# Optimization experiments

Measured on AMD Instinct MI355X. Metric: run time of the kernel, lower is better.

Reference implementation:

```python
import jax, jax.numpy as jnp
import numpy as np

D_IN = 1024
D_OUT = 1024


def setup_inputs() -> dict:
    key = jax.random.key(0)
    kx, kq, kk, kv = jax.random.split(key, 4)
    x = jax.random.normal(kx, (4, 2048, D_IN), dtype=jnp.float32)
    s = 1.0 / np.sqrt(D_IN)
    Wq = jax.random.normal(kq, (D_IN, D_OUT), dtype=jnp.float32) * s
    Wk = jax.random.normal(kk, (D_IN, D_OUT), dtype=jnp.float32) * s
    Wv = jax.random.normal(kv, (D_IN, D_OUT), dtype=jnp.float32) * s
    return {"x": x, "Wq": Wq, "Wk": Wk, "Wv": Wv}


def reference(x, Wq, Wk, Wv):
    # x: [B, S, d_in]; W*: [d_in, d_out]
    B, S, _ = x.shape
    q = x @ Wq  # [B, S, d_out]
    k = x @ Wk
    v = x @ Wv
    scale = 1.0 / jnp.sqrt(jnp.asarray(k.shape[-1], x.dtype))
    scores = jnp.einsum("bqd,bkd->bqk", q, k) * scale  # [B, S, S]
    # causal mask: positions j > i masked to -inf (triu, diagonal=1)
    causal = jnp.tril(jnp.ones((S, S), dtype=bool))
    scores = jnp.where(causal[None, :, :], scores, -jnp.inf)
    attn = jax.nn.softmax(scores, axis=-1)  # dropout p=0.0 -> identity
    return jnp.einsum("bqk,bkd->bqd", attn, v)
```

## Files before the change

kernel.cpp:

```cpp
#include <hip/hip_runtime.h>
#include <hip/hip_bf16.h>

#define NB 4
#define SB 2048
#define DD 1024
#define BM 128
#define BN 128
#define BK 32

typedef __attribute__((ext_vector_type(8))) short bf16x8;
typedef __attribute__((ext_vector_type(4))) short bf16x4;
typedef __attribute__((ext_vector_type(4))) float f32x4;
typedef unsigned int u32;

__device__ __forceinline__ float bf2f(unsigned short u) {
    return __uint_as_float(((u32)u) << 16);
}
__device__ __forceinline__ short f2bf(float f) {
    u32 u = __float_as_uint(f);
    u32 r = (u + 0x7fffu + ((u >> 16) & 1u)) >> 16;
    return (short)r;
}

__global__ __launch_bounds__(256) void prep(
    const float* __restrict__ x, const float* __restrict__ Wq,
    const float* __restrict__ Wk, const float* __restrict__ Wv,
    short* __restrict__ xb, short* __restrict__ Wqb,
    short* __restrict__ Wkb, short* __restrict__ Wvt)
{
    __shared__ short t[64][65];
    const int bx = blockIdx.x;
    const int tid = threadIdx.x;
    if (bx < 5120) {
        const float* src;
        short* dst;
        size_t i;
        if (bx < 4096) {
            src = x; dst = xb;
            i = ((size_t)bx * 256 + tid) * 8;
        } else {
            const int w = bx - 4096;
            src = (w < 512) ? Wq : Wk;
            dst = (w < 512) ? Wqb : Wkb;
            i = ((size_t)(w & 511) * 256 + tid) * 8;
        }
        float4 a = *(const float4*)&src[i];
        float4 b = *(const float4*)&src[i + 4];
        bf16x8 o;
        o[0] = f2bf(a.x); o[1] = f2bf(a.y); o[2] = f2bf(a.z); o[3] = f2bf(a.w);
        o[4] = f2bf(b.x); o[5] = f2bf(b.y); o[6] = f2bf(b.z); o[7] = f2bf(b.w);
        *(bf16x8*)&dst[i] = o;
        return;
    }
    const int rr = bx - 5120;
    const int k0 = (rr & 15) * 64;
    const int n0 = (rr >> 4) * 64;
    {
        const int r = tid >> 4;
        const int c = (tid & 15) * 4;
#pragma unroll
        for (int i = 0; i < 4; i++) {
            float4 v = *(const float4*)&Wv[(size_t)(k0 + i * 16 + r) * DD + n0 + c];
            t[i * 16 + r][c + 0] = f2bf(v.x);
            t[i * 16 + r][c + 1] = f2bf(v.y);
            t[i * 16 + r][c + 2] = f2bf(v.z);
            t[i * 16 + r][c + 3] = f2bf(v.w);
        }
    }
    __syncthreads();
    {
        const int r = tid >> 3;
        const int c = (tid & 7) * 8;
#pragma unroll
        for (int i = 0; i < 2; i++) {
            bf16x8 o;
#pragma unroll
            for (int j = 0; j < 8; j++) o[j] = t[c + j][i * 32 + r];
            *(bf16x8*)&Wvt[(size_t)(n0 + i * 32 + r) * DD + k0 + c] = o;
        }
    }
}

__device__ __forceinline__ void stage128x32(const short* __restrict__ g, int ld,
                                            short* lds, int tid) {
    const int wave = tid >> 6, lane = tid & 63;
    const int r = lane >> 2;
    const int c = (lane & 3) * 8;
#pragma unroll
    for (int i = 0; i < 2; i++) {
        const int chunk = wave * 2 + i;
        const short* gp = g + (size_t)(chunk * 16 + r) * ld + c;
        __builtin_amdgcn_global_load_lds(
            (const __attribute__((address_space(1))) u32*)gp,
            (__attribute__((address_space(3))) u32*)(lds + chunk * 512 + lane * 8),
            16, 0, 0);
    }
}

__device__ __forceinline__ void gemm_bt_body(
    const short* __restrict__ A, int lda, const short* __restrict__ Bt, int ldb,
    int m0, int n0, int kend, short* As, short* Bs, f32x4 (&acc)[4][4], int tid)
{
    const int lane = tid & 63;
    const int wave = tid >> 6;
    const int wm = (wave >> 1) * 64, wn = (wave & 1) * 64;
    const int fr = lane & 15;
    const int quad = lane >> 4;
    for (int k0 = 0; k0 < kend; k0 += BK) {
        stage128x32(A + (size_t)m0 * lda + k0, lda, As, tid);
        stage128x32(Bt + (size_t)n0 * ldb + k0, ldb, Bs, tid);
        __syncthreads();
        bf16x8 af[4], bf[4];
#pragma unroll
        for (int t = 0; t < 4; t++) {
            af[t] = *(const bf16x8*)&As[(wm + t * 16 + fr) * BK + quad * 8];
            bf[t] = *(const bf16x8*)&Bs[(wn + t * 16 + fr) * BK + quad * 8];
        }
#pragma unroll
        for (int mt = 0; mt < 4; mt++)
#pragma unroll
            for (int nt = 0; nt < 4; nt++)
                acc[mt][nt] = __builtin_amdgcn_mfma_f32_16x16x32_bf16(
                    af[mt], bf[nt], acc[mt][nt], 0, 0, 0);
        __syncthreads();
    }
}

__global__ __launch_bounds__(256) void mm_kernel(
    const short* __restrict__ Wkb, const short* __restrict__ Wqb,
    short* __restrict__ Mp)
{
    __shared__ short As[BM * BK], Bs[BN * BK];
    const int n0 = blockIdx.x * BN;
    const int m0 = blockIdx.y * BM;
    f32x4 acc[4][4];
#pragma unroll
    for (int a = 0; a < 4; a++)
#pragma unroll
        for (int b = 0; b < 4; b++) acc[a][b] = (f32x4){0.f, 0.f, 0.f, 0.f};
    gemm_bt_body(Wkb, DD, Wqb, DD, m0, n0, DD, As, Bs, acc, threadIdx.x);
    const int lane = threadIdx.x & 63, wave = threadIdx.x >> 6;
    const int wm = (wave >> 1) * 64, wn = (wave & 1) * 64;
    const int fr = lane & 15, quad = lane >> 4;
#pragma unroll
    for (int mt = 0; mt < 4; mt++)
#pragma unroll
        for (int nt = 0; nt < 4; nt++)
#pragma unroll
            for (int r = 0; r < 4; r++) {
                const size_t m = m0 + wm + mt * 16 + quad * 4 + r;
                const size_t n = n0 + wn + nt * 16 + fr;
                Mp[m * DD + n] = f2bf(acc[mt][nt][r]);
            }
}

__global__ __launch_bounds__(256) void tv_gemm(
    const short* __restrict__ xb, const short* __restrict__ Mp,
    const short* __restrict__ Wvt, short* __restrict__ T,
    short* __restrict__ Vt)
{
    __shared__ short As[BM * BK], Bs[BN * BK];
    const int n0 = blockIdx.x * BN;
    const int m0 = blockIdx.y * BM;
    const int z = blockIdx.z;
    const short* B = (z == 0) ? Mp : Wvt;
    f32x4 acc[4][4];
#pragma unroll
    for (int a = 0; a < 4; a++)
#pragma unroll
        for (int b = 0; b < 4; b++) acc[a][b] = (f32x4){0.f, 0.f, 0.f, 0.f};
    gemm_bt_body(xb, DD, B, DD, m0, n0, DD, As, Bs, acc, threadIdx.x);
    const int lane = threadIdx.x & 63, wave = threadIdx.x >> 6;
    const int wm = (wave >> 1) * 64, wn = (wave & 1) * 64;
    const int fr = lane & 15, quad = lane >> 4;
    if (z == 0) {
#pragma unroll
        for (int mt = 0; mt < 4; mt++)
#pragma unroll
            for (int nt = 0; nt < 4; nt++)
#pragma unroll
                for (int r = 0; r < 4; r++) {
                    const size_t m = m0 + wm + mt * 16 + quad * 4 + r;
                    const size_t n = n0 + wn + nt * 16 + fr;
                    T[m * DD + n] = f2bf(acc[mt][nt][r]);
                }
    } else {
        const int bb = m0 >> 11;
        const int s0 = (m0 & (SB - 1)) + wm + quad * 4;
        short* Vb = Vt + (size_t)bb * DD * SB;
#pragma unroll
        for (int mt = 0; mt < 4; mt++)
#pragma unroll
            for (int nt = 0; nt < 4; nt++) {
                const size_t n = n0 + wn + nt * 16 + fr;
                const size_t s = s0 + mt * 16;
                bf16x4 o;
#pragma unroll
                for (int r = 0; r < 4; r++) o[r] = f2bf(acc[mt][nt][r]);
                *(bf16x4*)&Vb[n * SB + s] = o;
            }
    }
}

__global__ __launch_bounds__(256) void scores_mfma(
    const short* __restrict__ T, const short* __restrict__ xb,
    short* __restrict__ Sc)
{
    const int idx = blockIdx.x;
    int qt = (int)((__fsqrt_rn(8.f * idx + 1.f) - 1.f) * 0.5f);
    while ((qt + 1) * (qt + 2) / 2 <= idx) qt++;
    while (qt * (qt + 1) / 2 > idx) qt--;
    const int kt = idx - qt * (qt + 1) / 2;
    const int qm0 = qt * BM;
    const int kn0 = kt * BN;
    const int b = blockIdx.y;
    __shared__ short As[BM * BK], Bs[BN * BK];
    const short* Tb = T + (size_t)b * SB * DD;
    const short* Xb = xb + (size_t)b * SB * DD;
    short* Sb = Sc + (size_t)b * SB * SB;
    f32x4 acc[4][4];
#pragma unroll
    for (int a = 0; a < 4; a++)
#pragma unroll
        for (int c = 0; c < 4; c++) acc[a][c] = (f32x4){0.f, 0.f, 0.f, 0.f};
    gemm_bt_body(Tb, DD, Xb, DD, qm0, kn0, DD, As, Bs, acc, threadIdx.x);
    const int lane = threadIdx.x & 63, wave = threadIdx.x >> 6;
    const int wm = (wave >> 1) * 64, wn = (wave & 1) * 64;
    const int fr = lane & 15, quad = lane >> 4;
    const float scale = 0.03125f;
#pragma unroll
    for (int mt = 0; mt < 4; mt++)
#pragma unroll
        for (int nt = 0; nt < 4; nt++)
#pragma unroll
            for (int r = 0; r < 4; r++) {
                const size_t q = qm0 + wm + mt * 16 + quad * 4 + r;
                const size_t k = kn0 + wn + nt * 16 + fr;
                Sb[q * SB + k] = f2bf(acc[mt][nt][r] * scale);
            }
}

__global__ __launch_bounds__(256) void softmax_kernel(short* __restrict__ Sc)
{
    const int row = blockIdx.x;
    const int i = row & (SB - 1);
    const int jlim = ((i >> 7) + 1) << 7;
    short* r = Sc + (size_t)row * SB;
    const int t = threadIdx.x;
    const int lane = t & 63, wave = t >> 6;
    __shared__ float red[8];

    float v[8];
    float mx = -1e30f;
#pragma unroll
    for (int c = 0; c < 8; c++) {
        const int j = c * 256 + t;
        const float s = (j <= i) ? bf2f((unsigned short)r[j]) : -1e30f;
        v[c] = s;
        mx = fmaxf(mx, s);
    }
#pragma unroll
    for (int o = 32; o > 0; o >>= 1) mx = fmaxf(mx, __shfl_down(mx, o));
    if (lane == 0) red[wave] = mx;
    __syncthreads();
    mx = fmaxf(fmaxf(red[0], red[1]), fmaxf(red[2], red[3]));

    float sum = 0.f;
#pragma unroll
    for (int c = 0; c < 8; c++) {
        const int j = c * 256 + t;
        const float e = (j <= i) ? __expf(v[c] - mx) : 0.f;
        v[c] = e;
        sum += e;
    }
#pragma unroll
    for (int o = 32; o > 0; o >>= 1) sum += __shfl_down(sum, o);
    if (lane == 0) red[4 + wave] = sum;
    __syncthreads();
    const float inv = 1.0f / (red[4] + red[5] + red[6] + red[7]);
#pragma unroll
    for (int c = 0; c < 8; c++) {
        const int j = c * 256 + t;
        if (j < jlim) r[j] = f2bf(v[c] * inv);
    }
}

__global__ __launch_bounds__(256) void pv_mfma(
    const short* __restrict__ P, const short* __restrict__ Vt,
    float* __restrict__ O, float* __restrict__ Pp)
{
    __shared__ short As[BM * BK], Bs[BN * BK];
    const int n0 = blockIdx.x * BN;
    const int y = blockIdx.y;
    const int chunk1 = (y >= 16);
    const int qt = chunk1 ? (y - 8) : y;
    const int qm0 = qt * BM;
    const int kstart = chunk1 ? 1024 : 0;
    const int kstop = chunk1 ? (qt + 1) * BM : min(1024, (qt + 1) * BM);
    const int b = blockIdx.z;
    const short* Pb = P + (size_t)b * SB * SB + kstart;
    const short* Vb = Vt + (size_t)b * DD * SB + kstart;
    f32x4 acc[4][4];
#pragma unroll
    for (int a = 0; a < 4; a++)
#pragma unroll
        for (int c = 0; c < 4; c++) acc[a][c] = (f32x4){0.f, 0.f, 0.f, 0.f};
    gemm_bt_body(Pb, SB, Vb, SB, qm0, n0, kstop - kstart, As, Bs, acc,
                 threadIdx.x);
    const int lane = threadIdx.x & 63, wave = threadIdx.x >> 6;
    const int wm = (wave >> 1) * 64, wn = (wave & 1) * 64;
    const int fr = lane & 15, quad = lane >> 4;
    float* dst = chunk1 ? (Pp + (size_t)b * 1024 * DD)
                        : (O + (size_t)b * SB * DD);
    const int qoff = chunk1 ? 1024 : 0;
#pragma unroll
    for (int mt = 0; mt < 4; mt++)
#pragma unroll
        for (int nt = 0; nt < 4; nt++)
#pragma unroll
            for (int r = 0; r < 4; r++) {
                const size_t q = qm0 + wm + mt * 16 + quad * 4 + r - qoff;
                const size_t n = n0 + wn + nt * 16 + fr;
                dst[q * DD + n] = acc[mt][nt][r];
            }
}

__global__ __launch_bounds__(256) void reduce_pv(const float* __restrict__ Pp,
                                                 float* __restrict__ O)
{
    const size_t e = ((size_t)blockIdx.x * 256 + threadIdx.x) * 4;
    const size_t b = e / ((size_t)1024 * DD);
    const size_t rem = e - b * (size_t)1024 * DD;
    float4 p = *(const float4*)&Pp[e];
    float* o = &O[b * (size_t)SB * DD + (size_t)1024 * DD + rem];
    float4 v = *(const float4*)o;
    v.x += p.x; v.y += p.y; v.z += p.z; v.w += p.w;
    *(float4*)o = v;
}

extern "C" void kernel_launch(void* const* d_in, const int* in_sizes, int n_in,
                              void* d_out, int out_size, void* d_ws, size_t ws_size,
                              hipStream_t stream)
{
    const float* x  = (const float*)d_in[0];
    const float* Wq = (const float*)d_in[1];
    const float* Wk = (const float*)d_in[2];
    const float* Wv = (const float*)d_in[3];
    float* out = (float*)d_out;

    const size_t XE = (size_t)NB * SB * DD;
    const size_t WE = (size_t)DD * DD;
    short* xb  = (short*)d_ws;
    short* T   = xb + XE;
    short* Vt  = T + XE;
    short* Sc  = Vt + XE;
    float* Pp  = (float*)(Sc + (size_t)NB * SB * SB);
    short* Wqb = (short*)(Pp + (size_t)NB * 1024 * DD);
    short* Wkb = Wqb + WE;
    short* Wvt = Wkb + WE;
    short* Mp  = Wvt + WE;

    prep<<<dim3(4096 + 1024 + 256), 256, 0, stream>>>(
        x, Wq, Wk, Wv, xb, Wqb, Wkb, Wvt);
    mm_kernel<<<dim3(DD / BN, DD / BM), 256, 0, stream>>>(Wkb, Wqb, Mp);
    tv_gemm<<<dim3(DD / BN, (NB * SB) / BM, 2), 256, 0, stream>>>(
        xb, Mp, Wvt, T, Vt);
    scores_mfma<<<dim3(136, NB), 256, 0, stream>>>(T, xb, Sc);
    softmax_kernel<<<dim3(NB * SB), 256, 0, stream>>>(Sc);
    pv_mfma<<<dim3(DD / BN, 24, NB), 256, 0, stream>>>(Sc, Vt, out, Pp);
    reduce_pv<<<dim3((unsigned)((size_t)NB * 1024 * DD / 4 / 256)), 256, 0,
                stream>>>(Pp, out);
}
```

Measured before the change: 271.3 us.

## Fuse Wk·Wqᵀ product into prep kernel and split T/V GEMMs

The Wk·Wqᵀ product is computed directly from fp32 weights inside the prep kernel, converting to bf16 while staging into LDS. This removes the separate bf16 conversion of Wq and Wk and the standalone mm_kernel launch. The combined T/V GEMM is split into two kernels, and the z-dependent branch in the epilogue goes away. The 64 GEMM blocks now run beside the conversion blocks inside one launch, so they may become a long tail. Staging fp32 through registers also replaces the direct global-to-LDS loads for that GEMM.

```diff
diff --git a/kernel.cpp b/kernel.cpp
--- a/kernel.cpp
+++ b/kernel.cpp
@@ -22,37 +22,125 @@
     return (short)r;
 }
 
-__global__ __launch_bounds__(256) void prep(
+__device__ __forceinline__ void mfma_step(const short* As, const short* Bs,
+                                          f32x4 (&acc)[4][4], int lane, int wave)
+{
+    const int wm = (wave >> 1) * 64, wn = (wave & 1) * 64;
+    const int fr = lane & 15;
+    const int quad = lane >> 4;
+    bf16x8 af[4], bf[4];
+#pragma unroll
+    for (int t = 0; t < 4; t++) {
+        af[t] = *(const bf16x8*)&As[(wm + t * 16 + fr) * BK + quad * 8];
+        bf[t] = *(const bf16x8*)&Bs[(wn + t * 16 + fr) * BK + quad * 8];
+    }
+#pragma unroll
+    for (int mt = 0; mt < 4; mt++)
+#pragma unroll
+        for (int nt = 0; nt < 4; nt++)
+            acc[mt][nt] = __builtin_amdgcn_mfma_f32_16x16x32_bf16(
+                af[mt], bf[nt], acc[mt][nt], 0, 0, 0);
+}
+
+__device__ __forceinline__ void stage128x32(const short* __restrict__ g, int ld,
+                                            short* lds, int tid) {
+    const int wave = tid >> 6, lane = tid & 63;
+    const int r = lane >> 2;
+    const int c = (lane & 3) * 8;
+#pragma unroll
+    for (int i = 0; i < 2; i++) {
+        const int chunk = wave * 2 + i;
+        const short* gp = g + (size_t)(chunk * 16 + r) * ld + c;
+        __builtin_amdgcn_global_load_lds(
+            (const __attribute__((address_space(1))) u32*)gp,
+            (__attribute__((address_space(3))) u32*)(lds + chunk * 512 + lane * 8),
+            16, 0, 0);
+    }
+}
+
+__device__ __forceinline__ void stage_f32_128x32(const float* __restrict__ g,
+                                                 int ld, short* lds, int tid) {
+    const int r = tid >> 1;
+    const int c = (tid & 1) * 16;
+    const float* gp = &g[(size_t)r * ld + c];
+    float4 v0 = *(const float4*)(gp + 0);
+    float4 v1 = *(const float4*)(gp + 4);
+    float4 v2 = *(const float4*)(gp + 8);
+    float4 v3 = *(const float4*)(gp + 12);
+    bf16x8 o0, o1;
+    o0[0] = f2bf(v0.x); o0[1] = f2bf(v0.y); o0[2] = f2bf(v0.z); o0[3] = f2bf(v0.w);
+    o0[4] = f2bf(v1.x); o0[5] = f2bf(v1.y); o0[6] = f2bf(v1.z); o0[7] = f2bf(v1.w);
+    o1[0] = f2bf(v2.x); o1[1] = f2bf(v2.y); o1[2] = f2bf(v2.z); o1[3] = f2bf(v2.w);
+    o1[4] = f2bf(v3.x); o1[5] = f2bf(v3.y); o1[6] = f2bf(v3.z); o1[7] = f2bf(v3.w);
+    *(bf16x8*)&lds[r * BK + c] = o0;
+    *(bf16x8*)&lds[r * BK + c + 8] = o1;
+}
+
+__device__ __forceinline__ void gemm_bt_body(
+    const short* __restrict__ A, int lda, const short* __restrict__ Bt, int ldb,
+    int m0, int n0, int kend, short* As, short* Bs, f32x4 (&acc)[4][4], int tid)
+{
+    const int lane = tid & 63;
+    const int wave = tid >> 6;
+    for (int k0 = 0; k0 < kend; k0 += BK) {
+        stage128x32(A + (size_t)m0 * lda + k0, lda, As, tid);
+        stage128x32(Bt + (size_t)n0 * ldb + k0, ldb, Bs, tid);
+        __syncthreads();
+        mfma_step(As, Bs, acc, lane, wave);
+        __syncthreads();
+    }
+}
+
+__global__ __launch_bounds__(256) void prep_mm(
     const float* __restrict__ x, const float* __restrict__ Wq,
     const float* __restrict__ Wk, const float* __restrict__ Wv,
-    short* __restrict__ xb, short* __restrict__ Wqb,
-    short* __restrict__ Wkb, short* __restrict__ Wvt)
-{
+    short* __restrict__ xb, short* __restrict__ Wvt, short* __restrict__ Mp)
+{
+    __shared__ short As[BM * BK], Bs[BN * BK];
     __shared__ short t[64][65];
     const int bx = blockIdx.x;
     const int tid = threadIdx.x;
-    if (bx < 5120) {
-        const float* src;
-        short* dst;
-        size_t i;
-        if (bx < 4096) {
-            src = x; dst = xb;
-            i = ((size_t)bx * 256 + tid) * 8;
-        } else {
-            const int w = bx - 4096;
-            src = (w < 512) ? Wq : Wk;
-            dst = (w < 512) ? Wqb : Wkb;
-            i = ((size_t)(w & 511) * 256 + tid) * 8;
+    if (bx < 64) {
+        const int m0 = (bx >> 3) * BM;
+        const int n0 = (bx & 7) * BN;
+        const int lane = tid & 63, wave = tid >> 6;
+        f32x4 acc[4][4];
+#pragma unroll
+        for (int a = 0; a < 4; a++)
+#pragma unroll
+            for (int b = 0; b < 4; b++) acc[a][b] = (f32x4){0.f, 0.f, 0.f, 0.f};
+        for (int k0 = 0; k0 < DD; k0 += BK) {
+            stage_f32_128x32(Wk + (size_t)m0 * DD + k0, DD, As, tid);
+            stage_f32_128x32(Wq + (size_t)n0 * DD + k0, DD, Bs, tid);
+            __syncthreads();
+            mfma_step(As, Bs, acc, lane, wave);
+            __syncthreads();
         }
-        float4 a = *(const float4*)&src[i];
-        float4 b = *(const float4*)&src[i + 4];
+        const int wm = (wave >> 1) * 64, wn = (wave & 1) * 64;
+        const int fr = lane & 15, quad = lane >> 4;
+#pragma unroll
+        for (int mt = 0; mt < 4; mt++)
+#pragma unroll
+            for (int nt = 0; nt < 4; nt++)
+#pragma unroll
+                for (int r = 0; r < 4; r++) {
+                    const size_t m = m0 + wm + mt * 16 + quad * 4 + r;
+                    const size_t n = n0 + wn + nt * 16 + fr;
+                    Mp[m * DD + n] = f2bf(acc[mt][nt][r]);
+                }
+        return;
+    }
+    if (bx < 4160) {
+        const size_t i = ((size_t)(bx - 64) * 256 + tid) * 8;
+        float4 a = *(const float4*)&x[i];
+        float4 b = *(const float4*)&x[i + 4];
         bf16x8 o;
         o[0] = f2bf(a.x); o[1] = f2bf(a.y); o[2] = f2bf(a.z); o[3] = f2bf(a.w);
         o[4] = f2bf(b.x); o[5] = f2bf(b.y); o[6] = f2bf(b.z); o[7] = f2bf(b.w);
-        *(bf16x8*)&dst[i] = o;
+        *(bf16x8*)&xb[i] = o;
         return;
     }
-    const int rr = bx - 5120;
+    const int rr = bx - 4160;
     const int k0 = (rr & 15) * 64;
     const int n0 = (rr >> 4) * 64;
     {
@@ -81,54 +169,9 @@
     }
 }
 
-__device__ __forceinline__ void stage128x32(const short* __restrict__ g, int ld,
-                                            short* lds, int tid) {
-    const int wave = tid >> 6, lane = tid & 63;
-    const int r = lane >> 2;
-    const int c = (lane & 3) * 8;
-#pragma unroll
-    for (int i = 0; i < 2; i++) {
-        const int chunk = wave * 2 + i;
-        const short* gp = g + (size_t)(chunk * 16 + r) * ld + c;
-        __builtin_amdgcn_global_load_lds(
-            (const __attribute__((address_space(1))) u32*)gp,
-            (__attribute__((address_space(3))) u32*)(lds + chunk * 512 + lane * 8),
-            16, 0, 0);
-    }
-}
-
-__device__ __forceinline__ void gemm_bt_body(
-    const short* __restrict__ A, int lda, const short* __restrict__ Bt, int ldb,
-    int m0, int n0, int kend, short* As, short* Bs, f32x4 (&acc)[4][4], int tid)
-{
-    const int lane = tid & 63;
-    const int wave = tid >> 6;
-    const int wm = (wave >> 1) * 64, wn = (wave & 1) * 64;
-    const int fr = lane & 15;
-    const int quad = lane >> 4;
-    for (int k0 = 0; k0 < kend; k0 += BK) {
-        stage128x32(A + (size_t)m0 * lda + k0, lda, As, tid);
-        stage128x32(Bt + (size_t)n0 * ldb + k0, ldb, Bs, tid);
-        __syncthreads();
-        bf16x8 af[4], bf[4];
-#pragma unroll
-        for (int t = 0; t < 4; t++) {
-            af[t] = *(const bf16x8*)&As[(wm + t * 16 + fr) * BK + quad * 8];
-            bf[t] = *(const bf16x8*)&Bs[(wn + t * 16 + fr) * BK + quad * 8];
-        }
-#pragma unroll
-        for (int mt = 0; mt < 4; mt++)
-#pragma unroll
-            for (int nt = 0; nt < 4; nt++)
-                acc[mt][nt] = __builtin_amdgcn_mfma_f32_16x16x32_bf16(
-                    af[mt], bf[nt], acc[mt][nt], 0, 0, 0);
-        __syncthreads();
-    }
-}
-
-__global__ __launch_bounds__(256) void mm_kernel(
-    const short* __restrict__ Wkb, const short* __restrict__ Wqb,
-    short* __restrict__ Mp)
+__global__ __launch_bounds__(256) void t_gemm(
+    const short* __restrict__ xb, const short* __restrict__ Mp,
+    short* __restrict__ T)
 {
     __shared__ short As[BM * BK], Bs[BN * BK];
     const int n0 = blockIdx.x * BN;
@@ -138,7 +181,7 @@
     for (int a = 0; a < 4; a++)
 #pragma unroll
         for (int b = 0; b < 4; b++) acc[a][b] = (f32x4){0.f, 0.f, 0.f, 0.f};
-    gemm_bt_body(Wkb, DD, Wqb, DD, m0, n0, DD, As, Bs, acc, threadIdx.x);
+    gemm_bt_body(xb, DD, Mp, DD, m0, n0, DD, As, Bs, acc, threadIdx.x);
     const int lane = threadIdx.x & 63, wave = threadIdx.x >> 6;
     const int wm = (wave >> 1) * 64, wn = (wave & 1) * 64;
     const int fr = lane & 15, quad = lane >> 4;
@@ -150,56 +193,40 @@
             for (int r = 0; r < 4; r++) {
                 const size_t m = m0 + wm + mt * 16 + quad * 4 + r;
                 const size_t n = n0 + wn + nt * 16 + fr;
-                Mp[m * DD + n] = f2bf(acc[mt][nt][r]);
+                T[m * DD + n] = f2bf(acc[mt][nt][r]);
             }
 }
 
-__global__ __launch_bounds__(256) void tv_gemm(
-    const short* __restrict__ xb, const short* __restrict__ Mp,
-    const short* __restrict__ Wvt, short* __restrict__ T,
+__global__ __launch_bounds__(256) void v_gemm(
+    const short* __restrict__ xb, const short* __restrict__ Wvt,
     short* __restrict__ Vt)
 {
     __shared__ short As[BM * BK], Bs[BN * BK];
     const int n0 = blockIdx.x * BN;
     const int m0 = blockIdx.y * BM;
-    const int z = blockIdx.z;
-    const short* B = (z == 0) ? Mp : Wvt;
     f32x4 acc[4][4];
 #pragma unroll
     for (int a = 0; a < 4; a++)
 #pragma unroll
         for (int b = 0; b < 4; b++) acc[a][b] = (f32x4){0.f, 0.f, 0.f, 0.f};
-    gemm_bt_body(xb, DD, B, DD, m0, n0, DD, As, Bs, acc, threadIdx.x);
+    gemm_bt_body(xb, DD, Wvt, DD, m0, n0, DD, As, Bs, acc, threadIdx.x);
     const int lane = threadIdx.x & 63, wave = threadIdx.x >> 6;
     const int wm = (wave >> 1) * 64, wn = (wave & 1) * 64;
     const int fr = lane & 15, quad = lane >> 4;
-    if (z == 0) {
-#pragma unroll
-        for (int mt = 0; mt < 4; mt++)
-#pragma unroll
-            for (int nt = 0; nt < 4; nt++)
-#pragma unroll
-                for (int r = 0; r < 4; r++) {
-                    const size_t m = m0 + wm + mt * 16 + quad * 4 + r;
-                    const size_t n = n0 + wn + nt * 16 + fr;
-                    T[m * DD + n] = f2bf(acc[mt][nt][r]);
-                }
-    } else {
-        const int bb = m0 >> 11;
-        const int s0 = (m0 & (SB - 1)) + wm + quad * 4;
-        short* Vb = Vt + (size_t)bb * DD * SB;
-#pragma unroll
-        for (int mt = 0; mt < 4; mt++)
-#pragma unroll
-            for (int nt = 0; nt < 4; nt++) {
-                const size_t n = n0 + wn + nt * 16 + fr;
-                const size_t s = s0 + mt * 16;
-                bf16x4 o;
-#pragma unroll
-                for (int r = 0; r < 4; r++) o[r] = f2bf(acc[mt][nt][r]);
-                *(bf16x4*)&Vb[n * SB + s] = o;
-            }
-    }
+    const int bb = m0 >> 11;
+    const int s0 = (m0 & (SB - 1)) + wm + quad * 4;
+    short* Vb = Vt + (size_t)bb * DD * SB;
+#pragma unroll
+    for (int mt = 0; mt < 4; mt++)
+#pragma unroll
+        for (int nt = 0; nt < 4; nt++) {
+            const size_t n = n0 + wn + nt * 16 + fr;
+            const size_t s = s0 + mt * 16;
+            bf16x4 o;
+#pragma unroll
+            for (int r = 0; r < 4; r++) o[r] = f2bf(acc[mt][nt][r]);
+            *(bf16x4*)&Vb[n * SB + s] = o;
+        }
 }
 
 __global__ __launch_bounds__(256) void scores_mfma(
@@ -355,16 +382,13 @@
     short* Vt  = T + XE;
     short* Sc  = Vt + XE;
     float* Pp  = (float*)(Sc + (size_t)NB * SB * SB);
-    short* Wqb = (short*)(Pp + (size_t)NB * 1024 * DD);
-    short* Wkb = Wqb + WE;
-    short* Wvt = Wkb + WE;
+    short* Wvt = (short*)(Pp + (size_t)NB * 1024 * DD);
     short* Mp  = Wvt + WE;
 
-    prep<<<dim3(4096 + 1024 + 256), 256, 0, stream>>>(
-        x, Wq, Wk, Wv, xb, Wqb, Wkb, Wvt);
-    mm_kernel<<<dim3(DD / BN, DD / BM), 256, 0, stream>>>(Wkb, Wqb, Mp);
-    tv_gemm<<<dim3(DD / BN, (NB * SB) / BM, 2), 256, 0, stream>>>(
-        xb, Mp, Wvt, T, Vt);
+    prep_mm<<<dim3(64 + 4096 + 256), 256, 0, stream>>>(
+        x, Wq, Wk, Wv, xb, Wvt, Mp);
+    t_gemm<<<dim3(DD / BN, (NB * SB) / BM), 256, 0, stream>>>(xb, Mp, T);
+    v_gemm<<<dim3(DD / BN, (NB * SB) / BM), 256, 0, stream>>>(xb, Wvt, Vt);
     scores_mfma<<<dim3(136, NB), 256, 0, stream>>>(T, xb, Sc);
     softmax_kernel<<<dim3(NB * SB), 256, 0, stream>>>(Sc);
     pv_mfma<<<dim3(DD / BN, 24, NB), 256, 0, stream>>>(Sc, Vt, out, Pp);
```

Measured after the change: 286.2 us. 1.05x slower.
